# Performance work log

Measured on AMD Instinct MI355X. Metric: run time of the kernel, lower is better.

## Reference

```python
import jax, jax.numpy as jnp
import numpy as np

SR = 44100
N_BINS = 84
BPO = 12
FMIN = 32.7
HOP = 1024


def _config():
    # Static CQT geometry (mirrors ICQT.__init__)
    Q = 1.0 / (2.0 ** (1.0 / BPO) - 1.0)
    freqs = FMIN * 2.0 ** (np.arange(N_BINS) / BPO)
    wlens = np.round(Q * SR / freqs).astype(np.int64)  # per-bin window lengths (ragged)
    return freqs, wlens


def setup_inputs() -> dict:
    key = jax.random.key(0)
    # complex CQT stacked as (nb_samples, nb_channels, n_bins, n_frames, 2)
    X = jax.random.normal(key, (4, 2, N_BINS, 256, 2), dtype=jnp.float32)
    return {"X": X}


def reference(X):
    freqs, wlens = _config()
    max_wl = int(wlens.max())
    nb_s, nb_c, n_bins, n_frames, _ = X.shape
    # default length in ICQT.forward when length is None
    length = (n_frames - 1) * HOP + max_wl

    Xf = X.reshape(-1, n_bins, n_frames, 2)
    c = (Xf[..., 0] + 1j * Xf[..., 1]).astype(jnp.complex64)  # view_as_complex
    B = c.shape[0]

    starts = np.arange(n_frames) * HOP  # static frame start times
    out = jnp.zeros((B, length), jnp.float32)
    norm_np = np.zeros(length, np.float32)  # norm is input-independent -> static numpy

    for k in range(n_bins):  # fixed structural loop over ragged bins
        L = int(wlens[k])
        t = np.arange(L)
        # torch.hann_window(L) (periodic)
        win = (0.5 - 0.5 * np.cos(2.0 * np.pi * t / L)).astype(np.float32)
        omega = 2.0 * np.pi * float(freqs[k]) / SR
        # exp(+1j*omega*t) * window, fused into one basis vector
        basis = jnp.asarray((np.exp(1j * omega * t) * win).astype(np.complex64))
        # frames: (B, n_frames, L) = outer product of per-frame coeff and basis
        frames = c[:, k, :, None] * basis[None, None, :]
        # vectorized overlap-add scatter (duplicate indices accumulate)
        idx = (starts[:, None] + t[None, :]).reshape(-1)  # (n_frames*L,)
        out = out.at[:, idx].add(jnp.real(frames).reshape(B, -1))
        np.add.at(norm_np, idx, np.tile(win * win, n_frames))

    norm = jnp.asarray(np.where(norm_np > 1e-10, norm_np, 1.0).astype(np.float32))
    out = out / norm[None, :]
    return out.reshape(nb_s, nb_c, -1)
```

## Files before the change

### kernel.cpp

```cpp
#include <hip/hip_runtime.h>
#include <hip/hip_fp16.h>
#include <cmath>

#define NBINS   84
#define NFRAMES 256
#define HOP     1024
#define NB      8
#define KP      960
#define KPH     (KP/2)
#define GBLK    278
#define MROWS   (GBLK*NB)
#define MPAD    2240
#define SD      23

#define BT_BLOCKS  2048
#define A_BLOCKS   (2*MPAD)
#define S_BLOCKS   92
#define ALL_BLOCKS (BT_BLOCKS + A_BLOCKS + S_BLOCKS)

typedef _Float16 f16x8 __attribute__((ext_vector_type(8)));
typedef float    f32x4 __attribute__((ext_vector_type(4)));

struct CqtArgs {
    int   wl[NBINS];
    float omega[NBINS];
    float invL[NBINS];
    int   Ktot;
    unsigned short ct[KP];
};

__global__ __launch_bounds__(256)
void mega_build(unsigned short* __restrict__ Am, unsigned short* __restrict__ Bt,
                float* __restrict__ S, const float* __restrict__ X, CqtArgs a) {
    const int blk = blockIdx.x;
    const int tid = threadIdx.x;
    const float TWOPI = 6.28318530717958647692f;

    if (blk < BT_BLOCKS) {
        const int r = blk >> 1;
        const int j = (blk & 1) * 256 + tid;
        if (j >= KPH) return;
        unsigned int pack = 0;
        const unsigned short rec = a.ct[2 * j];
        if (rec != 0xFFFF) {
            const int k = rec & 0x7F, d = (rec >> 7) & 0x1F;
            const int t = (d << 10) + r;
            if (t < a.wl[k]) {
                const float tf = (float)t;
                const float w  = 0.5f - 0.5f * cosf(TWOPI * tf * a.invL[k]);
                float s, c;
                sincosf(a.omega[k] * tf, &s, &c);
                pack = (unsigned int)__half_as_ushort(__float2half(c * w))
                     | ((unsigned int)__half_as_ushort(__float2half(s * w)) << 16);
            }
        }
        *(unsigned int*)(Bt + (size_t)r * KP + 2 * j) = pack;
    } else if (blk < BT_BLOCKS + A_BLOCKS) {
        const int idx = blk - BT_BLOCKS;
        const int row = idx >> 1;
        const int j   = (idx & 1) * 256 + tid;
        if (j >= KPH) return;
        unsigned int pack = 0;
        const unsigned short rec = a.ct[2 * j];
        if (row < MROWS && rec != 0xFFFF) {
            const int k = rec & 0x7F, d = (rec >> 7) & 0x1F;
            const int g = row >> 3, b = row & 7;
            const int f = g - d;
            if (f >= 0 && f < NFRAMES) {
                const float2 x = *(const float2*)(X + (((size_t)b * NBINS + k) * NFRAMES + f) * 2);
                pack = (unsigned int)__half_as_ushort(__float2half(x.x))
                     | ((unsigned int)__half_as_ushort(__float2half(-x.y)) << 16);
            }
        }
        *(unsigned int*)(Am + (size_t)row * KP + 2 * j) = pack;
    } else {
        const int t = (blk - BT_BLOCKS - A_BLOCKS) * 256 + tid;
        float sum = 0.f;
        for (int k = 0; k < NBINS; ++k) {
            if (t >= a.wl[k]) break;
            const float w = 0.5f - 0.5f * cosf(TWOPI * (float)t * a.invL[k]);
            sum += w * w;
        }
        S[t] = sum;
    }
}

__device__ __forceinline__ float inv_norm(const float* __restrict__ S, int g, int ncol) {
    if (g >= GBLK) return 1.0f;
    const int lo = (g > NFRAMES - 1) ? (g - (NFRAMES - 1)) : 0;
    const int hi = g < (SD - 1) ? g : (SD - 1);
    float s = 0.f;
    for (int d = lo; d <= hi; ++d) s += S[(d << 10) + ncol];
    return (s > 1e-10f) ? 1.0f / s : 1.0f;
}

__global__ __launch_bounds__(256)
void gemm_icqt(const unsigned short* __restrict__ Am, const unsigned short* __restrict__ Bt,
               const float* __restrict__ S, float* __restrict__ out, int length) {
    __shared__ __align__(16) char lds[16384];
    const int tid = threadIdx.x;
    const int l   = tid & 63;
    const int wid = tid >> 6;
    const int wm  = wid >> 1, wn = wid & 1;
    const int bm  = blockIdx.x, bn = blockIdx.y;

    const int q0 = tid,      q1 = tid + 256;
    const int r0 = q0 >> 3,  c0 = q0 & 7, s0 = c0 ^ (r0 & 7);
    const int r1 = q1 >> 3,  c1 = q1 & 7, s1 = c1 ^ (r1 & 7);

    const char* gA = (const char*)Am + (size_t)(bm * 64) * KP * 2;
    const char* gB = (const char*)Bt + (size_t)(bn * 64) * KP * 2;
    const char* gA0 = gA + ((size_t)r0 * KP + s0 * 8) * 2;
    const char* gA1 = gA + ((size_t)r1 * KP + s1 * 8) * 2;
    const char* gB0 = gB + ((size_t)r0 * KP + s0 * 8) * 2;
    const char* gB1 = gB + ((size_t)r1 * KP + s1 * 8) * 2;
    char* lA = lds;
    char* lB = lds + 8192;

    f32x4 acc00 = {0.f,0.f,0.f,0.f}, acc01 = {0.f,0.f,0.f,0.f};
    f32x4 acc10 = {0.f,0.f,0.f,0.f}, acc11 = {0.f,0.f,0.f,0.f};

    f16x8 ra0 = *(const f16x8*)(gA0);
    f16x8 ra1 = *(const f16x8*)(gA1);
    f16x8 rb0 = *(const f16x8*)(gB0);
    f16x8 rb1 = *(const f16x8*)(gB1);

    const int arow0 = wm * 32 + (l & 15), arow1 = arow0 + 16;
    const int brow0 = wn * 32 + (l & 15), brow1 = brow0 + 16;
    const int kq = l >> 4;

    for (int kk = 0; kk < KP; kk += 64) {
        __syncthreads();
        *(f16x8*)(lA + q0 * 16) = ra0;
        *(f16x8*)(lA + q1 * 16) = ra1;
        *(f16x8*)(lB + q0 * 16) = rb0;
        *(f16x8*)(lB + q1 * 16) = rb1;
        __syncthreads();
        if (kk + 64 < KP) {
            ra0 = *(const f16x8*)(gA0 + (kk + 64) * 2);
            ra1 = *(const f16x8*)(gA1 + (kk + 64) * 2);
            rb0 = *(const f16x8*)(gB0 + (kk + 64) * 2);
            rb1 = *(const f16x8*)(gB1 + (kk + 64) * 2);
        }
#pragma unroll
        for (int ks = 0; ks < 2; ++ks) {
            const int kb = ks * 4 + kq;
            f16x8 a0 = *(const f16x8*)(lA + arow0 * 128 + ((kb ^ (arow0 & 7)) << 4));
            f16x8 a1 = *(const f16x8*)(lA + arow1 * 128 + ((kb ^ (arow1 & 7)) << 4));
            f16x8 b0 = *(const f16x8*)(lB + brow0 * 128 + ((kb ^ (brow0 & 7)) << 4));
            f16x8 b1 = *(const f16x8*)(lB + brow1 * 128 + ((kb ^ (brow1 & 7)) << 4));
            acc00 = __builtin_amdgcn_mfma_f32_16x16x32_f16(a0, b0, acc00, 0, 0, 0);
            acc01 = __builtin_amdgcn_mfma_f32_16x16x32_f16(a0, b1, acc01, 0, 0, 0);
            acc10 = __builtin_amdgcn_mfma_f32_16x16x32_f16(a1, b0, acc10, 0, 0, 0);
            acc11 = __builtin_amdgcn_mfma_f32_16x16x32_f16(a1, b1, acc11, 0, 0, 0);
        }
    }

    const int mbase = bm * 64 + wm * 32;
    const int nbase = bn * 64 + wn * 32;
    const int ncol0 = nbase + (l & 15);
    const int ncol1 = ncol0 + 16;
    const int g0    = (mbase >> 3) + (kq >> 1);
    const float inv00 = inv_norm(S, g0,     ncol0);
    const float inv01 = inv_norm(S, g0,     ncol1);
    const float inv10 = inv_norm(S, g0 + 2, ncol0);
    const float inv11 = inv_norm(S, g0 + 2, ncol1);

#pragma unroll
    for (int mi = 0; mi < 2; ++mi) {
#pragma unroll
        for (int ni = 0; ni < 2; ++ni) {
            f32x4 v = (mi == 0) ? ((ni == 0) ? acc00 : acc01)
                                : ((ni == 0) ? acc10 : acc11);
            const float invv = (mi == 0) ? ((ni == 0) ? inv00 : inv01)
                                         : ((ni == 0) ? inv10 : inv11);
            const int ncol = (ni == 0) ? ncol0 : ncol1;
#pragma unroll
            for (int reg = 0; reg < 4; ++reg) {
                const int mrow = mbase + mi * 16 + kq * 4 + reg;
                if (mrow < MROWS) {
                    const int g = mrow >> 3, b = mrow & 7;
                    const int p = (g << 10) + ncol;
                    if (p < length)
                        out[(size_t)b * length + p] = v[reg] * invv;
                }
            }
        }
    }
}

__global__ void icqt_gather_fallback(const float* __restrict__ X, float* __restrict__ out,
                                     CqtArgs a, int length) {
    const int p = blockIdx.x * blockDim.x + threadIdx.x;
    if (p >= length) return;
    float acc[NB];
#pragma unroll
    for (int b = 0; b < NB; ++b) acc[b] = 0.0f;
    float nrm = 0.0f;
    int fhi = p >> 10;
    if (fhi > NFRAMES - 1) fhi = NFRAMES - 1;
    const float2* X2 = reinterpret_cast<const float2*>(X);
    for (int k = 0; k < NBINS; ++k) {
        const int L = a.wl[k];
        int flo = (p - L + HOP) >> 10;
        if (flo < 0) flo = 0;
        for (int f = flo; f <= fhi; ++f) {
            const int t = p - (f << 10);
            if (t < L) {
                float tf = (float)t;
                float ang = a.omega[k] * tf;
                float s = sinf(ang), c = cosf(ang);
                float w = 0.5f - 0.5f * cosf(6.28318530717958647692f * tf * a.invL[k]);
                float bre = c * w, bim = s * w;
                nrm += w * w;
                const int base = k * NFRAMES + f;
#pragma unroll
                for (int b = 0; b < NB; ++b) {
                    float2 cv = X2[(size_t)b * (NBINS * NFRAMES) + base];
                    acc[b] += cv.x * bre - cv.y * bim;
                }
            }
        }
    }
    const float inv = 1.0f / ((nrm > 1e-10f) ? nrm : 1.0f);
#pragma unroll
    for (int b = 0; b < NB; ++b)
        out[(size_t)b * length + p] = acc[b] * inv;
}

extern "C" void kernel_launch(void* const* d_in, const int* in_sizes, int n_in,
                              void* d_out, int out_size, void* d_ws, size_t ws_size,
                              hipStream_t stream) {
    CqtArgs a;
    int cb[NBINS];
    const double SR = 44100.0;
    const double Q  = 1.0 / (std::exp2(1.0 / 12.0) - 1.0);
    int Ktot = 0;
    for (int k = 0; k < NBINS; ++k) {
        double f = 32.7 * std::exp2((double)k / 12.0);
        int L = (int)std::nearbyint(Q * SR / f);
        a.wl[k]    = L;
        cb[k]      = Ktot;
        a.omega[k] = (float)(2.0 * 3.14159265358979323846 * f / SR);
        a.invL[k]  = (float)(1.0 / (double)L);
        Ktot += 2 * ((L + 1023) / 1024);
    }
    a.Ktot = Ktot;
    for (int col = 0; col < KP; ++col) a.ct[col] = 0xFFFF;
    if (Ktot <= KP) {
        for (int k = 0; k < NBINS; ++k) {
            const int D2 = 2 * ((a.wl[k] + 1023) / 1024);
            for (int j = 0; j < D2; ++j)
                a.ct[cb[k] + j] = (unsigned short)(k | ((j >> 1) << 7) | ((j & 1) << 12));
        }
    }

    const int length = out_size / NB;
    const float* X = (const float*)d_in[0];
    float* out     = (float*)d_out;

    const size_t offA = 0;
    const size_t szA  = (size_t)MPAD * KP * 2;
    const size_t offB = offA + szA;
    const size_t szB  = (size_t)1024 * KP * 2;
    const size_t offS = offB + szB;
    const size_t szS  = (size_t)SD * 1024 * 4;
    const size_t need = offS + szS;

    if (Ktot > KP || a.wl[0] > SD * 1024 || ws_size < need) {
        const int blocks = (length + 255) / 256;
        icqt_gather_fallback<<<blocks, 256, 0, stream>>>(X, out, a, length);
        return;
    }

    unsigned short* Am = (unsigned short*)((char*)d_ws + offA);
    unsigned short* Bt = (unsigned short*)((char*)d_ws + offB);
    float*          S  = (float*)((char*)d_ws + offS);

    mega_build<<<dim3(ALL_BLOCKS), 256, 0, stream>>>(Am, Bt, S, X, a);
    gemm_icqt<<<dim3(MPAD / 64, 1024 / 64), 256, 0, stream>>>(Am, Bt, S, out, length);
}
```

Baseline: 53.29 us.

## Fuse build and GEMM into one cooperative kernel with grid sync

Merges the operand-build kernel and the GEMM into a single cooperative launch of 560 blocks. Each block first runs grid-stride loops to build the fp16 basis, coefficient matrix and window-energy table, then waits at a grid-wide barrier and computes one 64x64 GEMM tile. The goal is to remove the second kernel launch and the gap between the two kernels. In exchange it adds a grid barrier, fewer build threads each doing more work with integer divides, and an occupancy hint of 3 blocks per SM. If the cooperative launch fails it falls back to the two separate kernels.

```diff
diff --git a/kernel.cpp b/kernel.cpp
--- a/kernel.cpp
+++ b/kernel.cpp
@@ -1,6 +1,9 @@
 #include <hip/hip_runtime.h>
 #include <hip/hip_fp16.h>
+#include <hip/hip_cooperative_groups.h>
 #include <cmath>
+
+namespace cg = cooperative_groups;
 
 #define NBINS   84
 #define NFRAMES 256
@@ -13,10 +16,8 @@
 #define MPAD    2240
 #define SD      23
 
-#define BT_BLOCKS  2048
-#define A_BLOCKS   (2*MPAD)
-#define S_BLOCKS   92
-#define ALL_BLOCKS (BT_BLOCKS + A_BLOCKS + S_BLOCKS)
+#define GRID_BLKS 560
+#define NTHREADS  (GRID_BLKS*256)
 
 typedef _Float16 f16x8 __attribute__((ext_vector_type(8)));
 typedef float    f32x4 __attribute__((ext_vector_type(4)));
@@ -29,17 +30,14 @@
     unsigned short ct[KP];
 };
 
-__global__ __launch_bounds__(256)
-void mega_build(unsigned short* __restrict__ Am, unsigned short* __restrict__ Bt,
-                float* __restrict__ S, const float* __restrict__ X, CqtArgs a) {
-    const int blk = blockIdx.x;
-    const int tid = threadIdx.x;
+__device__ __forceinline__ void build_all(unsigned short* __restrict__ Am,
+                                          unsigned short* __restrict__ Bt,
+                                          float* __restrict__ S,
+                                          const float* __restrict__ X,
+                                          const CqtArgs& a, int gtid) {
     const float TWOPI = 6.28318530717958647692f;
-
-    if (blk < BT_BLOCKS) {
-        const int r = blk >> 1;
-        const int j = (blk & 1) * 256 + tid;
-        if (j >= KPH) return;
+    for (int i = gtid; i < 1024 * KPH; i += NTHREADS) {
+        const int r = i / KPH, j = i - r * KPH;
         unsigned int pack = 0;
         const unsigned short rec = a.ct[2 * j];
         if (rec != 0xFFFF) {
@@ -55,11 +53,9 @@
             }
         }
         *(unsigned int*)(Bt + (size_t)r * KP + 2 * j) = pack;
-    } else if (blk < BT_BLOCKS + A_BLOCKS) {
-        const int idx = blk - BT_BLOCKS;
-        const int row = idx >> 1;
-        const int j   = (idx & 1) * 256 + tid;
-        if (j >= KPH) return;
+    }
+    for (int i = gtid; i < MPAD * KPH; i += NTHREADS) {
+        const int row = i / KPH, j = i - row * KPH;
         unsigned int pack = 0;
         const unsigned short rec = a.ct[2 * j];
         if (row < MROWS && rec != 0xFFFF) {
@@ -73,8 +69,8 @@
             }
         }
         *(unsigned int*)(Am + (size_t)row * KP + 2 * j) = pack;
-    } else {
-        const int t = (blk - BT_BLOCKS - A_BLOCKS) * 256 + tid;
+    }
+    for (int t = gtid; t < SD * 1024; t += NTHREADS) {
         float sum = 0.f;
         for (int k = 0; k < NBINS; ++k) {
             if (t >= a.wl[k]) break;
@@ -94,15 +90,16 @@
     return (s > 1e-10f) ? 1.0f / s : 1.0f;
 }
 
-__global__ __launch_bounds__(256)
-void gemm_icqt(const unsigned short* __restrict__ Am, const unsigned short* __restrict__ Bt,
-               const float* __restrict__ S, float* __restrict__ out, int length) {
+__device__ __forceinline__ void gemm_body(const unsigned short* __restrict__ Am,
+                                          const unsigned short* __restrict__ Bt,
+                                          const float* __restrict__ S,
+                                          float* __restrict__ out, int length,
+                                          int bm, int bn) {
     __shared__ __align__(16) char lds[16384];
     const int tid = threadIdx.x;
     const int l   = tid & 63;
     const int wid = tid >> 6;
     const int wm  = wid >> 1, wn = wid & 1;
-    const int bm  = blockIdx.x, bn = blockIdx.y;
 
     const int q0 = tid,      q1 = tid + 256;
     const int r0 = q0 >> 3,  c0 = q0 & 7, s0 = c0 ^ (r0 & 7);
@@ -187,6 +184,27 @@
             }
         }
     }
+}
+
+__global__ __launch_bounds__(256, 3)
+void icqt_coop(unsigned short* __restrict__ Am, unsigned short* __restrict__ Bt,
+               float* __restrict__ S, const float* __restrict__ X,
+               float* __restrict__ out, int length, CqtArgs a) {
+    build_all(Am, Bt, S, X, a, blockIdx.x * 256 + threadIdx.x);
+    cg::this_grid().sync();
+    gemm_body(Am, Bt, S, out, length, blockIdx.x >> 4, blockIdx.x & 15);
+}
+
+__global__ __launch_bounds__(256)
+void mega_build(unsigned short* __restrict__ Am, unsigned short* __restrict__ Bt,
+                float* __restrict__ S, const float* __restrict__ X, CqtArgs a) {
+    build_all(Am, Bt, S, X, a, blockIdx.x * 256 + threadIdx.x);
+}
+
+__global__ __launch_bounds__(256)
+void gemm_icqt(const unsigned short* __restrict__ Am, const unsigned short* __restrict__ Bt,
+               const float* __restrict__ S, float* __restrict__ out, int length) {
+    gemm_body(Am, Bt, S, out, length, blockIdx.x, blockIdx.y);
 }
 
 __global__ void icqt_gather_fallback(const float* __restrict__ X, float* __restrict__ out,
@@ -277,6 +295,14 @@
     unsigned short* Bt = (unsigned short*)((char*)d_ws + offB);
     float*          S  = (float*)((char*)d_ws + offS);
 
-    mega_build<<<dim3(ALL_BLOCKS), 256, 0, stream>>>(Am, Bt, S, X, a);
-    gemm_icqt<<<dim3(MPAD / 64, 1024 / 64), 256, 0, stream>>>(Am, Bt, S, out, length);
-}
+    int len_ = length;
+    void* kargs[] = { (void*)&Am, (void*)&Bt, (void*)&S, (void*)&X,
+                      (void*)&out, (void*)&len_, (void*)&a };
+    hipError_t ce = hipLaunchCooperativeKernel(icqt_coop, dim3(GRID_BLKS), dim3(256),
+                                               kargs, 0, stream);
+    if (ce != hipSuccess) {
+        (void)hipGetLastError();
+        mega_build<<<dim3((MPAD * KPH + 255) / 256 > 0 ? 6620 : 6620), 256, 0, stream>>>(Am, Bt, S, X, a);
+        gemm_icqt<<<dim3(MPAD / 64, 1024 / 64), 256, 0, stream>>>(Am, Bt, S, out, length);
+    }
+}
```

Result: slower. 111.1 us (+108.4%).

## Gather A operand directly from X inside GEMM instead of materializing it

Applied to the files above, without the earlier changes.

Removes the separate A-matrix build pass and its workspace buffer: the GEMM now gathers the Toeplitz-like A tiles straight from X on the fly, using the column table passed as a kernel argument. The Bt build is also vectorized so each thread writes 8 halves (16 bytes) instead of 2. This saves a global write and read of the roughly 4 MB A matrix. In exchange the GEMM inner loop performs scattered 8-byte loads and per-element index decoding, which may add latency to the main loop.

```diff
diff --git a/kernel.cpp b/kernel.cpp
--- a/kernel.cpp
+++ b/kernel.cpp
@@ -8,73 +8,63 @@
 #define NB      8
 #define KP      960
 #define KPH     (KP/2)
+#define KPQ     (KP/8)
 #define GBLK    278
 #define MROWS   (GBLK*NB)
 #define MPAD    2240
 #define SD      23
 
-#define BT_BLOCKS  2048
-#define A_BLOCKS   (2*MPAD)
+#define BT_BLOCKS  480
 #define S_BLOCKS   92
-#define ALL_BLOCKS (BT_BLOCKS + A_BLOCKS + S_BLOCKS)
+#define ALL_BLOCKS (BT_BLOCKS + S_BLOCKS)
 
 typedef _Float16 f16x8 __attribute__((ext_vector_type(8)));
 typedef float    f32x4 __attribute__((ext_vector_type(4)));
 
-struct CqtArgs {
+struct alignas(16) CqtArgs {
+    unsigned short ct[KP];
     int   wl[NBINS];
     float omega[NBINS];
     float invL[NBINS];
     int   Ktot;
-    unsigned short ct[KP];
 };
 
 __global__ __launch_bounds__(256)
-void mega_build(unsigned short* __restrict__ Am, unsigned short* __restrict__ Bt,
-                float* __restrict__ S, const float* __restrict__ X, CqtArgs a) {
+void build_bt_s(unsigned short* __restrict__ Bt, float* __restrict__ S, CqtArgs a) {
     const int blk = blockIdx.x;
     const int tid = threadIdx.x;
     const float TWOPI = 6.28318530717958647692f;
 
     if (blk < BT_BLOCKS) {
-        const int r = blk >> 1;
-        const int j = (blk & 1) * 256 + tid;
-        if (j >= KPH) return;
-        unsigned int pack = 0;
-        const unsigned short rec = a.ct[2 * j];
-        if (rec != 0xFFFF) {
-            const int k = rec & 0x7F, d = (rec >> 7) & 0x1F;
-            const int t = (d << 10) + r;
-            if (t < a.wl[k]) {
-                const float tf = (float)t;
-                const float w  = 0.5f - 0.5f * cosf(TWOPI * tf * a.invL[k]);
-                float s, c;
-                sincosf(a.omega[k] * tf, &s, &c);
-                pack = (unsigned int)__half_as_ushort(__float2half(c * w))
-                     | ((unsigned int)__half_as_ushort(__float2half(s * w)) << 16);
+        const int idx  = blk * 256 + tid;
+        const int r    = idx / KPQ;
+        const int quad = idx - r * KPQ;
+        const int jb   = quad * 4;
+        const uint4 rr = *(const uint4*)(&a.ct[2 * jb]);
+        const unsigned int recs[4] = { rr.x & 0xFFFFu, rr.y & 0xFFFFu,
+                                       rr.z & 0xFFFFu, rr.w & 0xFFFFu };
+        f16x8 v;
+#pragma unroll
+        for (int jj = 0; jj < 4; ++jj) {
+            float vc = 0.f, vs = 0.f;
+            const unsigned int rec = recs[jj];
+            if (rec != 0xFFFFu) {
+                const int k = rec & 0x7F, d = (rec >> 7) & 0x1F;
+                const int t = (d << 10) + r;
+                if (t < a.wl[k]) {
+                    const float tf = (float)t;
+                    const float w  = 0.5f - 0.5f * cosf(TWOPI * tf * a.invL[k]);
+                    float s, c;
+                    sincosf(a.omega[k] * tf, &s, &c);
+                    vc = c * w; vs = s * w;
+                }
             }
-        }
-        *(unsigned int*)(Bt + (size_t)r * KP + 2 * j) = pack;
-    } else if (blk < BT_BLOCKS + A_BLOCKS) {
-        const int idx = blk - BT_BLOCKS;
-        const int row = idx >> 1;
-        const int j   = (idx & 1) * 256 + tid;
-        if (j >= KPH) return;
-        unsigned int pack = 0;
-        const unsigned short rec = a.ct[2 * j];
-        if (row < MROWS && rec != 0xFFFF) {
-            const int k = rec & 0x7F, d = (rec >> 7) & 0x1F;
-            const int g = row >> 3, b = row & 7;
-            const int f = g - d;
-            if (f >= 0 && f < NFRAMES) {
-                const float2 x = *(const float2*)(X + (((size_t)b * NBINS + k) * NFRAMES + f) * 2);
-                pack = (unsigned int)__half_as_ushort(__float2half(x.x))
-                     | ((unsigned int)__half_as_ushort(__float2half(-x.y)) << 16);
-            }
-        }
-        *(unsigned int*)(Am + (size_t)row * KP + 2 * j) = pack;
+            v[2 * jj]     = (_Float16)vc;
+            v[2 * jj + 1] = (_Float16)vs;
+        }
+        *(f16x8*)(Bt + (size_t)r * KP + 8 * quad) = v;
     } else {
-        const int t = (blk - BT_BLOCKS - A_BLOCKS) * 256 + tid;
+        const int t = (blk - BT_BLOCKS) * 256 + tid;
         float sum = 0.f;
         for (int k = 0; k < NBINS; ++k) {
             if (t >= a.wl[k]) break;
@@ -94,9 +84,34 @@
     return (s > 1e-10f) ? 1.0f / s : 1.0f;
 }
 
+__device__ __forceinline__ f16x8 gather_A(const float2* __restrict__ X2,
+                                          const CqtArgs& a, int mrow, int jgbase) {
+    const int g = mrow >> 3, b = mrow & 7;
+    const bool rowok = (mrow < MROWS);
+    const uint4 rr = *(const uint4*)(&a.ct[2 * jgbase]);
+    const unsigned int recs[4] = { rr.x & 0xFFFFu, rr.y & 0xFFFFu,
+                                   rr.z & 0xFFFFu, rr.w & 0xFFFFu };
+    f16x8 v;
+#pragma unroll
+    for (int jj = 0; jj < 4; ++jj) {
+        float re = 0.f, nim = 0.f;
+        const unsigned int rec = recs[jj];
+        const int k = rec & 0x7F, d = (rec >> 7) & 0x1F;
+        const int f = g - d;
+        if (rowok && rec != 0xFFFFu && f >= 0 && f < NFRAMES) {
+            const float2 x = X2[((size_t)b * NBINS + k) * NFRAMES + f];
+            re = x.x; nim = -x.y;
+        }
+        v[2 * jj]     = (_Float16)re;
+        v[2 * jj + 1] = (_Float16)nim;
+    }
+    return v;
+}
+
 __global__ __launch_bounds__(256)
-void gemm_icqt(const unsigned short* __restrict__ Am, const unsigned short* __restrict__ Bt,
-               const float* __restrict__ S, float* __restrict__ out, int length) {
+void gemm_icqt(const float2* __restrict__ X2, const unsigned short* __restrict__ Bt,
+               const float* __restrict__ S, float* __restrict__ out, int length,
+               CqtArgs a) {
     __shared__ __align__(16) char lds[16384];
     const int tid = threadIdx.x;
     const int l   = tid & 63;
@@ -108,10 +123,10 @@
     const int r0 = q0 >> 3,  c0 = q0 & 7, s0 = c0 ^ (r0 & 7);
     const int r1 = q1 >> 3,  c1 = q1 & 7, s1 = c1 ^ (r1 & 7);
 
-    const char* gA = (const char*)Am + (size_t)(bm * 64) * KP * 2;
+    const int mrow0 = bm * 64 + r0;
+    const int mrow1 = bm * 64 + r1;
+
     const char* gB = (const char*)Bt + (size_t)(bn * 64) * KP * 2;
-    const char* gA0 = gA + ((size_t)r0 * KP + s0 * 8) * 2;
-    const char* gA1 = gA + ((size_t)r1 * KP + s1 * 8) * 2;
     const char* gB0 = gB + ((size_t)r0 * KP + s0 * 8) * 2;
     const char* gB1 = gB + ((size_t)r1 * KP + s1 * 8) * 2;
     char* lA = lds;
@@ -120,8 +135,8 @@
     f32x4 acc00 = {0.f,0.f,0.f,0.f}, acc01 = {0.f,0.f,0.f,0.f};
     f32x4 acc10 = {0.f,0.f,0.f,0.f}, acc11 = {0.f,0.f,0.f,0.f};
 
-    f16x8 ra0 = *(const f16x8*)(gA0);
-    f16x8 ra1 = *(const f16x8*)(gA1);
+    f16x8 ra0 = gather_A(X2, a, mrow0, s0 * 4);
+    f16x8 ra1 = gather_A(X2, a, mrow1, s1 * 4);
     f16x8 rb0 = *(const f16x8*)(gB0);
     f16x8 rb1 = *(const f16x8*)(gB1);
 
@@ -137,8 +152,9 @@
         *(f16x8*)(lB + q1 * 16) = rb1;
         __syncthreads();
         if (kk + 64 < KP) {
-            ra0 = *(const f16x8*)(gA0 + (kk + 64) * 2);
-            ra1 = *(const f16x8*)(gA1 + (kk + 64) * 2);
+            const int jgb = (kk + 64) >> 1;
+            ra0 = gather_A(X2, a, mrow0, jgb + s0 * 4);
+            ra1 = gather_A(X2, a, mrow1, jgb + s1 * 4);
             rb0 = *(const f16x8*)(gB0 + (kk + 64) * 2);
             rb1 = *(const f16x8*)(gB1 + (kk + 64) * 2);
         }
@@ -259,9 +275,7 @@
     const float* X = (const float*)d_in[0];
     float* out     = (float*)d_out;
 
-    const size_t offA = 0;
-    const size_t szA  = (size_t)MPAD * KP * 2;
-    const size_t offB = offA + szA;
+    const size_t offB = 0;
     const size_t szB  = (size_t)1024 * KP * 2;
     const size_t offS = offB + szB;
     const size_t szS  = (size_t)SD * 1024 * 4;
@@ -273,10 +287,10 @@
         return;
     }
 
-    unsigned short* Am = (unsigned short*)((char*)d_ws + offA);
     unsigned short* Bt = (unsigned short*)((char*)d_ws + offB);
     float*          S  = (float*)((char*)d_ws + offS);
 
-    mega_build<<<dim3(ALL_BLOCKS), 256, 0, stream>>>(Am, Bt, S, X, a);
-    gemm_icqt<<<dim3(MPAD / 64, 1024 / 64), 256, 0, stream>>>(Am, Bt, S, out, length);
-}
+    build_bt_s<<<dim3(ALL_BLOCKS), 256, 0, stream>>>(Bt, S, a);
+    gemm_icqt<<<dim3(MPAD / 64, 1024 / 64), 256, 0, stream>>>(
+        (const float2*)X, Bt, S, out, length, a);
+}
```

Result: slower. 68.60 us (+28.7%).
